# Kernel optimization log

Hardware: AMD Instinct MI355X
Metric: run time of the kernel (lower is better)

The kernel has to match this reference:

```python
import jax, jax.numpy as jnp
import numpy as np

L, B, S, D = 8, 1, 4096, 2048
H, KVH, HD = 16, 2, 128
Q = 32
THETA = 1e6
MROPE = (16, 24, 24)  # mrope_section, sums to HD//2
EPS = 1e-6


def setup_inputs() -> dict:
    key = jax.random.key(0)
    ks = jax.random.split(key, 8)
    hidden_states = jax.random.normal(ks[0], (L, B, S, D), dtype=jnp.float32)
    ln_w = jax.random.uniform(ks[1], (L, D), dtype=jnp.float32, minval=0.5, maxval=1.5)
    q_w = jax.random.normal(ks[2], (L, D, H * HD), dtype=jnp.float32) * 0.02
    q_b = jax.random.normal(ks[3], (L, H * HD), dtype=jnp.float32) * 0.02
    k_w = jax.random.normal(ks[4], (L, D, KVH * HD), dtype=jnp.float32) * 0.02
    k_b = jax.random.normal(ks[5], (L, KVH * HD), dtype=jnp.float32) * 0.02
    position_ids = jax.random.randint(ks[6], (3, B, S), 0, S, dtype=jnp.int32)
    q_idx = jnp.sort(jax.random.randint(ks[7], (Q,), 0, S, dtype=jnp.int32))
    return {"hidden_states": hidden_states, "ln_w": ln_w, "q_w": q_w, "q_b": q_b,
            "k_w": k_w, "k_b": k_b, "position_ids": position_ids, "q_idx": q_idx}


def _rot_half(x):
    h = x.shape[-1] // 2
    return jnp.concatenate([-x[..., h:], x[..., :h]], axis=-1)


def _mrope_combine(t):
    # t: (3, B, S, HD). Split last dim per 2*mrope_section, chunk i taken from axis i%3.
    parts, off = [], 0
    for i, sec in enumerate(MROPE):
        w = 2 * sec
        parts.append(t[i % 3, :, :, off:off + w])
        off += w
    return jnp.concatenate(parts, axis=-1)[:, None, :, :]  # (B, 1, S, HD)


def reference(hidden_states, ln_w, q_w, q_b, k_w, k_b, position_ids, q_idx):
    # Rotary embeddings from 3D mRoPE position ids
    inv_freq = 1.0 / (THETA ** (jnp.arange(0, HD, 2, dtype=jnp.float32) / HD))  # (HD/2,)
    freqs = position_ids.astype(jnp.float32)[..., None] * inv_freq  # (3, B, S, HD/2)
    emb = jnp.concatenate([freqs, freqs], axis=-1)  # (3, B, S, HD)
    cos = _mrope_combine(jnp.cos(emb))  # (B, 1, S, HD)
    sin = _mrope_combine(jnp.sin(emb))
    cos_q = cos[:, :, q_idx, :]  # (B, 1, Q, HD)
    sin_q = sin[:, :, q_idx, :]
    # Eager causal mask sliced at query rows: (Q, S)
    mask_add = jnp.where(jnp.arange(S)[None, :] > q_idx[:, None], -1e9, 0.0).astype(jnp.float32)

    scale = 1.0 / np.sqrt(HD).astype(np.float32)

    def per_layer(hs, lw, qw, qb, kw, kb):
        # RMSNorm (input_layernorm)
        var = jnp.mean(jnp.square(hs), axis=-1, keepdims=True)
        x = hs * jax.lax.rsqrt(var + EPS) * lw  # (B, S, D)
        xq = x[:, q_idx, :]  # (B, Q, D)
        k = (jnp.einsum('bsd,de->bse', x, kw) + kb).reshape(B, S, KVH, HD).transpose(0, 2, 1, 3)
        q = (jnp.einsum('bqd,de->bqe', xq, qw) + qb).reshape(B, Q, H, HD).transpose(0, 2, 1, 3)
        k = jnp.repeat(k, H // KVH, axis=1)  # repeat_kv -> (B, H, S, HD)
        k = k * cos + _rot_half(k) * sin
        q = q * cos_q + _rot_half(q) * sin_q
        scores = jnp.einsum('bhqd,bhkd->bhqk', q, k) * scale  # (B, H, Q, S)
        scores = scores + mask_add[None, None]
        return jax.nn.softmax(scores.astype(jnp.float32), axis=-1)

    return jax.vmap(per_layer)(hidden_states, ln_w, q_w, q_b, k_w, k_b)  # (L, B, H, Q, S)
```

## Files before the change

kernel.cpp:

```cpp
#include <hip/hip_runtime.h>
#include <hip/hip_bf16.h>
#include <math.h>

#define LYR 8
#define SEQ 4096
#define DIM 2048
#define NH 16
#define HD 128
#define NQ 32
#define NKV 256
#define NQE 2048

typedef __attribute__((ext_vector_type(8))) short short8;
typedef __attribute__((ext_vector_type(4))) float f32x4;

#define WS_IRQ   0
#define WS_ABLOB 256
#define WS_COS   524544
#define WS_SIN   1048832
#define WS_QBUF  1573120
#define WS_PART  2097408
#define WS_W2    4194560
#define WS_KBLOB 8388864
#define WS_QBLOB 16777472

__device__ __forceinline__ short f2bf(float x) {
  __hip_bfloat16 h = __float2bfloat16(x);
  return *(short*)&h;
}
__device__ __forceinline__ float bf2f(short s) {
  unsigned u = ((unsigned)(unsigned short)s) << 16;
  return __uint_as_float(u);
}

__device__ __forceinline__ void split1(float x, short& h, short& l) {
  unsigned b = __float_as_uint(x);
  h = (short)(b >> 16);
  float lo = x - __uint_as_float(b & 0xffff0000u);
  l = (short)((__float_as_uint(lo) + 0x8000u) >> 16);
}

#define GLOAD16(srcp, dstp) \
  __builtin_amdgcn_global_load_lds( \
      (const __attribute__((address_space(1))) unsigned int*)(srcp), \
      (__attribute__((address_space(3))) unsigned int*)(dstp), 16, 0, 0)

#define RBAR() asm volatile("s_waitcnt lgkmcnt(0)\n\ts_barrier" ::: "memory")

__global__ __launch_bounds__(256) void prep_kernel(
    const float* __restrict__ ln_w, const float* __restrict__ k_w,
    short* __restrict__ W2) {
  int kb = blockIdx.x, l = blockIdx.y, t = threadIdx.x;
  const float* kwl = k_w + (size_t)l * DIM * NKV;
  const float* lnl = ln_w + l * DIM;
  short* blob = W2 + (size_t)(l * 64 + kb) * 16384;
  #pragma unroll
  for (int i = 0; i < 4; ++i) {
    int p = t + i * 256;
    int fi = p >> 6, lane = p & 63;
    int n = fi * 16 + (lane & 15);
    int k0 = kb * 32 + (lane >> 4) * 8;
    short hi8[8], lo8[8];
    #pragma unroll
    for (int e = 0; e < 8; ++e) {
      float v = lnl[k0 + e] * kwl[(size_t)(k0 + e) * NKV + n];
      short h = f2bf(v);
      hi8[e] = h;
      lo8[e] = f2bf(v - bf2f(h));
    }
    *(short8*)(blob + p * 8) = *(short8*)hi8;
    *(short8*)(blob + 8192 + p * 8) = *(short8*)lo8;
  }
}

__global__ __launch_bounds__(256) void rmsq_kernel(const float* __restrict__ hs,
                                                   const int* __restrict__ q_idx,
                                                   float* __restrict__ irq) {
  int qi = blockIdx.x, l = blockIdx.y, t = threadIdx.x;
  int s = q_idx[qi];
  const float* row = hs + ((size_t)l * SEQ + s) * DIM;
  float4 v0 = *(const float4*)(row + t * 4);
  float4 v1 = *(const float4*)(row + t * 4 + 1024);
  float acc = v0.x*v0.x + v0.y*v0.y + v0.z*v0.z + v0.w*v0.w
            + v1.x*v1.x + v1.y*v1.y + v1.z*v1.z + v1.w*v1.w;
  #pragma unroll
  for (int off = 32; off >= 1; off >>= 1) acc += __shfl_down(acc, off);
  __shared__ float red[4];
  if ((t & 63) == 0) red[t >> 6] = acc;
  __syncthreads();
  if (t == 0) {
    float tot = red[0] + red[1] + red[2] + red[3];
    irq[l * NQ + qi] = rsqrtf(tot / (float)DIM + 1e-6f);
  }
}

__global__ void cossin_kernel(const int* __restrict__ pos_ids,
                              float* __restrict__ cost, float* __restrict__ sint) {
  int idx = blockIdx.x * 256 + threadIdx.x;
  int s = idx >> 7, d = idx & 127;
  int t = (d < 32) ? 0 : (d < 80 ? 1 : 2);
  int j = d & 63;
  double invf = pow(1000000.0, -(double)j / 64.0);
  double ph = (double)pos_ids[t * SEQ + s] * invf;
  cost[idx] = (float)cos(ph);
  sint[idx] = (float)sin(ph);
}

__global__ __launch_bounds__(256) void xqt_kernel(
    const float* __restrict__ hs, const float* __restrict__ ln_w,
    const int* __restrict__ q_idx, const float* __restrict__ irq,
    short* __restrict__ Ablob) {
  __shared__ int qix[32];
  __shared__ float qir[32];
  int l = blockIdx.x, t = threadIdx.x;
  if (t < 32) { qix[t] = q_idx[t]; qir[t] = irq[l * NQ + t]; }
  __syncthreads();
  int lane = t & 63, g4 = t >> 6;
  short* base = Ablob + (size_t)l * 131072;
  int row = lane & 15, kgl = lane >> 4;
  for (int i = 0; i < 64; ++i) {
    int group = g4 * 64 + i;
    int kb = group >> 2, half = (group >> 1) & 1, mf = group & 1;
    int r = row + mf * 16;
    int k0 = kb * 32 + kgl * 8;
    const float* src = hs + ((size_t)l * SEQ + qix[r]) * DIM + k0;
    const float* lnp = ln_w + l * DIM + k0;
    float ir = qir[r];
    float4 v0 = *(const float4*)src;
    float4 v1 = *(const float4*)(src + 4);
    float4 w0 = *(const float4*)lnp;
    float4 w1 = *(const float4*)(lnp + 4);
    float av[8] = {v0.x*w0.x, v0.y*w0.y, v0.z*w0.z, v0.w*w0.w,
                   v1.x*w1.x, v1.y*w1.y, v1.z*w1.z, v1.w*w1.w};
    short o8[8];
    #pragma unroll
    for (int e = 0; e < 8; ++e) {
      float v = av[e] * ir;
      short hh, ll;
      split1(v, hh, ll);
      o8[e] = half ? ll : hh;
    }
    *(short8*)(base + group * 512 + lane * 8) = *(short8*)o8;
  }
}

__global__ __launch_bounds__(256) void kgemm_kernel(
    const float* __restrict__ hs, const short* __restrict__ W2,
    const float* __restrict__ k_b, const float* __restrict__ cost,
    const float* __restrict__ sint, short* __restrict__ Kblob) {
  __shared__ __align__(1024) char SM[65536];

  int t = threadIdx.x;
  int fid = blockIdx.x;
  int l = fid & 7, sb = fid >> 3;
  int s0 = sb * 64;
  int lane = t & 63, w = t >> 6;
  int fr = lane & 15, kg = lane >> 4;
  int arow = t >> 2, akg = t & 3;

  const float* hrow = hs + ((size_t)l * SEQ + s0 + arow) * DIM + akg * 8;
  const char* wbase = (const char*)(W2 + (size_t)l * 64 * 16384);
  const char* wfrag = wbase + w * 1024 + lane * 16;

  int awoff = (arow >> 4) * 1024 + (((akg * 16 + (arow & 15)) * 16) ^ (akg << 5));
  int aroff = (lane * 16) ^ ((lane >> 4) << 5);

  f32x4 acc[4][4];
  #pragma unroll
  for (int mf = 0; mf < 4; ++mf)
    #pragma unroll
    for (int nf = 0; nf < 4; ++nf) acc[mf][nf] = (f32x4){0.f, 0.f, 0.f, 0.f};
  float sq = 0.f;
  float4 rA0, rA1, rB0, rB1;
  short8 B0h[4], B0l[4], B1h[4], B1l[4];

  {
    #pragma unroll
    for (int nf = 0; nf < 4; ++nf) {
      B0h[nf] = *(const short8*)(wfrag + nf * 4096);
      B0l[nf] = *(const short8*)(wfrag + nf * 4096 + 16384);
    }
    float4 a0 = *(const float4*)(hrow);
    float4 a1 = *(const float4*)(hrow + 4);
    float av[8] = {a0.x, a0.y, a0.z, a0.w, a1.x, a1.y, a1.z, a1.w};
    short hi8[8], lo8[8];
    #pragma unroll
    for (int e = 0; e < 8; ++e) {
      sq = fmaf(av[e], av[e], sq);
      split1(av[e], hi8[e], lo8[e]);
    }
    *(short8*)(SM + awoff) = *(short8*)hi8;
    *(short8*)(SM + 4096 + awoff) = *(short8*)lo8;
    rA0 = *(const float4*)(hrow + 32);
    rA1 = *(const float4*)(hrow + 36);
  }
  RBAR();

#define KSTEP8(KB, CA0, CA1, NA0, NA1, UBH, UBL, PBH, PBL) do { \
    int buf_ = (KB) & 1; \
    const char* asb_ = SM + buf_ * 8192; \
     \
    if ((KB) < 63) { \
      const char* bsrc_ = wfrag + (size_t)((KB) + 1) * 32768; \
      _Pragma("unroll") \
      for (int nf = 0; nf < 4; ++nf) { \
        PBH[nf] = *(const short8*)(bsrc_ + nf * 4096); \
        PBL[nf] = *(const short8*)(bsrc_ + nf * 4096 + 16384); \
      } \
    } \
    if ((KB) < 62) { \
      NA0 = *(const float4*)(hrow + ((KB) + 2) * 32); \
      NA1 = *(const float4*)(hrow + ((KB) + 2) * 32 + 4); \
    } \
    short8 ah_[4], al_[4]; \
    _Pragma("unroll") \
    for (int mf = 0; mf < 4; ++mf) { \
      ah_[mf] = *(const short8*)(asb_ + mf * 1024 + aroff); \
      al_[mf] = *(const short8*)(asb_ + 4096 + mf * 1024 + aroff); \
    } \
    __builtin_amdgcn_s_barrier(); \
    asm volatile("s_waitcnt lgkmcnt(0)" ::: "memory"); \
    __builtin_amdgcn_s_setprio(1); \
    _Pragma("unroll") \
    for (int nf = 0; nf < 2; ++nf) \
      _Pragma("unroll") \
      for (int mf = 0; mf < 4; ++mf) \
        acc[mf][nf] = __builtin_amdgcn_mfma_f32_16x16x32_bf16(ah_[mf], UBH[nf], acc[mf][nf], 0, 0, 0); \
    _Pragma("unroll") \
    for (int nf = 0; nf < 2; ++nf) \
      _Pragma("unroll") \
      for (int mf = 0; mf < 4; ++mf) \
        acc[mf][nf] = __builtin_amdgcn_mfma_f32_16x16x32_bf16(ah_[mf], UBL[nf], acc[mf][nf], 0, 0, 0); \
    _Pragma("unroll") \
    for (int nf = 0; nf < 2; ++nf) \
      _Pragma("unroll") \
      for (int mf = 0; mf < 4; ++mf) \
        acc[mf][nf] = __builtin_amdgcn_mfma_f32_16x16x32_bf16(al_[mf], UBH[nf], acc[mf][nf], 0, 0, 0); \
    __builtin_amdgcn_s_setprio(0); \
    __builtin_amdgcn_s_barrier(); \
     \
    if ((KB) < 63) { \
      char* asn_ = SM + (buf_ ^ 1) * 8192; \
      float av_[8] = {CA0.x, CA0.y, CA0.z, CA0.w, CA1.x, CA1.y, CA1.z, CA1.w}; \
      short hi8_[8], lo8_[8]; \
      _Pragma("unroll") \
      for (int e = 0; e < 8; ++e) { \
        sq = fmaf(av_[e], av_[e], sq); \
        split1(av_[e], hi8_[e], lo8_[e]); \
      } \
      *(short8*)(asn_ + awoff) = *(short8*)hi8_; \
      *(short8*)(asn_ + 4096 + awoff) = *(short8*)lo8_; \
    } \
    __builtin_amdgcn_s_setprio(1); \
    _Pragma("unroll") \
    for (int nf = 2; nf < 4; ++nf) \
      _Pragma("unroll") \
      for (int mf = 0; mf < 4; ++mf) \
        acc[mf][nf] = __builtin_amdgcn_mfma_f32_16x16x32_bf16(ah_[mf], UBH[nf], acc[mf][nf], 0, 0, 0); \
    _Pragma("unroll") \
    for (int nf = 2; nf < 4; ++nf) \
      _Pragma("unroll") \
      for (int mf = 0; mf < 4; ++mf) \
        acc[mf][nf] = __builtin_amdgcn_mfma_f32_16x16x32_bf16(ah_[mf], UBL[nf], acc[mf][nf], 0, 0, 0); \
    _Pragma("unroll") \
    for (int nf = 2; nf < 4; ++nf) \
      _Pragma("unroll") \
      for (int mf = 0; mf < 4; ++mf) \
        acc[mf][nf] = __builtin_amdgcn_mfma_f32_16x16x32_bf16(al_[mf], UBH[nf], acc[mf][nf], 0, 0, 0); \
    __builtin_amdgcn_s_setprio(0); \
    asm volatile("s_waitcnt lgkmcnt(0)" ::: "memory"); \
    __builtin_amdgcn_s_barrier(); \
  } while (0)

  for (int kb2 = 0; kb2 < 32; ++kb2) {
    KSTEP8(2 * kb2,     rA0, rA1, rB0, rB1, B0h, B0l, B1h, B1l);
    KSTEP8(2 * kb2 + 1, rB0, rB1, rA0, rA1, B1h, B1l, B0h, B0l);
  }
#undef KSTEP8

  sq += __shfl_xor(sq, 1);
  sq += __shfl_xor(sq, 2);
  float* smf = (float*)SM;
  __syncthreads();
  if ((t & 3) == 0) smf[arow] = sq;
  __syncthreads();
  float irv[16];
  #pragma unroll
  for (int mf = 0; mf < 4; ++mf)
    #pragma unroll
    for (int r = 0; r < 4; ++r)
      irv[mf * 4 + r] = rsqrtf(smf[mf * 16 + kg * 4 + r] / (float)DIM + 1e-6f);
  __syncthreads();

  float* Kraw = smf;
  int j = w * 16 + fr;
  float bias0 = k_b[l * NKV + j];
  float bias1 = k_b[l * NKV + j + 64];
  float bias2 = k_b[l * NKV + j + 128];
  float bias3 = k_b[l * NKV + j + 192];
  #pragma unroll
  for (int mf = 0; mf < 4; ++mf) {
    #pragma unroll
    for (int r = 0; r < 4; ++r) {
      int row = mf * 16 + kg * 4 + r;
      int s = s0 + row;
      float ir = irv[mf * 4 + r];
      float v0 = acc[mf][0][r] * ir + bias0;
      float v1 = acc[mf][1][r] * ir + bias1;
      float v2 = acc[mf][2][r] * ir + bias2;
      float v3 = acc[mf][3][r] * ir + bias3;
      float cj = cost[s * HD + j], sj = sint[s * HD + j];
      float cj2 = cost[s * HD + j + 64], sj2 = sint[s * HD + j + 64];
      int sw = (row & 7) << 2;
      float* kr = Kraw + row * 256;
      kr[j ^ sw]           = v0 * cj - v1 * sj;
      kr[(j + 64) ^ sw]    = v1 * cj2 + v0 * sj2;
      kr[(j + 128) ^ sw]   = v2 * cj - v3 * sj;
      kr[(j + 192) ^ sw]   = v3 * cj2 + v2 * sj2;
    }
  }
  __syncthreads();

  int kc = sb >> 1, fb = (sb & 1) * 4;
  #pragma unroll
  for (int i = 0; i < 8; ++i) {
    int c = t + i * 256;
    int lc = c & 63, fl = (c >> 6) & 3, ts2 = (c >> 8) & 3, kv = c >> 10;
    int key = fl * 16 + (lc & 15);
    int d0 = kv * 128 + ts2 * 32 + (lc >> 4) * 8;
    int sw = (key & 7) << 2;
    float4 x0 = *(const float4*)(Kraw + key * 256 + (d0 ^ sw));
    float4 x1 = *(const float4*)(Kraw + key * 256 + ((d0 + 4) ^ sw));
    float av[8] = {x0.x, x0.y, x0.z, x0.w, x1.x, x1.y, x1.z, x1.w};
    short hi8[8], lo8[8];
    #pragma unroll
    for (int e = 0; e < 8; ++e) split1(av[e], hi8[e], lo8[e]);
    short* bb = Kblob + (size_t)((l * 2 + kv) * 32 + kc) * 32768
              + (size_t)((ts2 * 2 + 0) * 8 + fb + fl) * 512 + lc * 8;
    *(short8*)bb = *(short8*)hi8;
    *(short8*)(bb + 4096) = *(short8*)lo8;
  }
}

__global__ __launch_bounds__(512) void qgemm_kernel(
    const float* __restrict__ q_w, const short* __restrict__ Ablob,
    float* __restrict__ part) {
  __shared__ __align__(1024) char SM[131072];
  int t = threadIdx.x;
  int nc = blockIdx.x, ks = blockIdx.y, l = blockIdx.z;
  int lane = t & 63, w = t >> 6;
  int fr = lane & 15, kg = lane >> 4;
  const char* abase = (const char*)(Ablob + (size_t)l * 131072 + (size_t)ks * 32768);
  const float* qwl = q_w + (size_t)l * DIM * NQE;

  #pragma unroll
  for (int c = 0; c < 8; ++c) {
    int chunk = w * 8 + c;
    GLOAD16(abase + chunk * 1024 + lane * 16, SM + chunk * 1024);
  }
  #pragma unroll
  for (int c = 0; c < 4; ++c) {
    int r = w * 4 + c;
    GLOAD16((const char*)(qwl + (size_t)(ks * 512 + r) * NQE + nc * 256) + lane * 16,
            SM + 65536 + r * 1024 + lane * 16);
  }
  f32x4 acc[2][2];
  #pragma unroll
  for (int mf = 0; mf < 2; ++mf)
    #pragma unroll
    for (int nf = 0; nf < 2; ++nf) acc[mf][nf] = (f32x4){0.f, 0.f, 0.f, 0.f};
  __syncthreads();

  for (int ts = 0; ts < 16; ++ts) {
    int buf = ts & 1;
    if (ts < 15) {
      #pragma unroll
      for (int c = 0; c < 4; ++c) {
        int r = w * 4 + c;
        GLOAD16((const char*)(qwl + (size_t)(ks * 512 + (ts + 1) * 32 + r) * NQE + nc * 256) + lane * 16,
                SM + 65536 + (buf ^ 1) * 32768 + r * 1024 + lane * 16);
      }
    }
    short8 ah[2], al[2];
    #pragma unroll
    for (int mf = 0; mf < 2; ++mf) {
      ah[mf] = *(const short8*)(SM + ts * 4096 + mf * 1024 + lane * 16);
      al[mf] = *(const short8*)(SM + ts * 4096 + 2048 + mf * 1024 + lane * 16);
    }
    const float* bt = (const float*)(SM + 65536 + buf * 32768);
    short8 bh[2], bl[2];
    #pragma unroll
    for (int nf = 0; nf < 2; ++nf) {
      int c = w * 32 + nf * 16 + fr;
      short bh8[8], bl8[8];
      #pragma unroll
      for (int e = 0; e < 8; ++e) {
        float v = bt[(kg * 8 + e) * 256 + c];
        split1(v, bh8[e], bl8[e]);
      }
      bh[nf] = *(short8*)bh8;
      bl[nf] = *(short8*)bl8;
    }
    #pragma unroll
    for (int nf = 0; nf < 2; ++nf)
      #pragma unroll
      for (int mf = 0; mf < 2; ++mf)
        acc[mf][nf] = __builtin_amdgcn_mfma_f32_16x16x32_bf16(ah[mf], bh[nf], acc[mf][nf], 0, 0, 0);
    #pragma unroll
    for (int nf = 0; nf < 2; ++nf)
      #pragma unroll
      for (int mf = 0; mf < 2; ++mf)
        acc[mf][nf] = __builtin_amdgcn_mfma_f32_16x16x32_bf16(ah[mf], bl[nf], acc[mf][nf], 0, 0, 0);
    #pragma unroll
    for (int nf = 0; nf < 2; ++nf)
      #pragma unroll
      for (int mf = 0; mf < 2; ++mf)
        acc[mf][nf] = __builtin_amdgcn_mfma_f32_16x16x32_bf16(al[mf], bh[nf], acc[mf][nf], 0, 0, 0);
    __syncthreads();
  }

  #pragma unroll
  for (int mf = 0; mf < 2; ++mf) {
    #pragma unroll
    for (int r = 0; r < 4; ++r) {
      int row = mf * 16 + kg * 4 + r;
      float* prow = part + ((size_t)((ks * LYR + l) * NQ + row)) * NQE + nc * 256;
      #pragma unroll
      for (int nf = 0; nf < 2; ++nf) {
        int col = w * 32 + nf * 16 + fr;
        prow[col] = acc[mf][nf][r];
      }
    }
  }
}

__global__ __launch_bounds__(256) void qred_kernel(
    const float* __restrict__ part, const float* __restrict__ q_b,
    float* __restrict__ Qbuf) {
  int idx = blockIdx.x * 256 + threadIdx.x;
  int n = idx & 2047, q = (idx >> 11) & 31, l = idx >> 16;
  float v = q_b[l * NQE + n];
  #pragma unroll
  for (int ks = 0; ks < 4; ++ks)
    v += part[((size_t)((ks * LYR + l) * NQ + q)) * NQE + n];
  Qbuf[((size_t)l * NQ + q) * NQE + n] = v;
}

__global__ __launch_bounds__(256) void qpack_kernel(
    const float* __restrict__ Qbuf, const float* __restrict__ cost,
    const float* __restrict__ sint, const int* __restrict__ q_idx,
    short* __restrict__ Qblob) {
  int kv = blockIdx.x, l = blockIdx.y, t = threadIdx.x;
  short* blob = Qblob + (size_t)(l * 2 + kv) * 65536;
  #pragma unroll
  for (int i = 0; i < 16; ++i) {
    int p = t + i * 256;
    int ts = p >> 10, f = (p >> 6) & 15, lane = p & 63;
    int row = f * 16 + (lane & 15);
    int hh = row >> 5, q = row & 31;
    int h = kv * 8 + hh;
    int d0 = ts * 32 + (lane >> 4) * 8;
    int s = q_idx[q];
    const float* qrow = Qbuf + ((size_t)l * NQ + q) * NQE + h * HD;
    const float* ct = cost + s * HD;
    const float* st = sint + s * HD;
    short hi8[8], lo8[8];
    #pragma unroll
    for (int e = 0; e < 8; ++e) {
      int d = d0 + e;
      float x = qrow[d];
      float xp = qrow[d ^ 64];
      float v = (d < 64) ? (x * ct[d] - xp * st[d]) : (x * ct[d] + xp * st[d]);
      split1(v, hi8[e], lo8[e]);
    }
    *(short8*)(blob + ((ts * 2 + 0) * 16 + f) * 512 + lane * 8) = *(short8*)hi8;
    *(short8*)(blob + ((ts * 2 + 1) * 16 + f) * 512 + lane * 8) = *(short8*)lo8;
  }
}

__global__ __launch_bounds__(512) void scores_kernel(
    const short* __restrict__ Qblob, const short* __restrict__ Kblob,
    const int* __restrict__ q_idx, float* __restrict__ out) {
  __shared__ short Qs[2][16384];
  __shared__ short Ks[2][8192];
  __shared__ int qiv[32];
  int t = threadIdx.x;
  int kc = blockIdx.x, kv = blockIdx.y, l = blockIdx.z;
  int lane = t & 63, w = t >> 6;
  int wm = w >> 1, wn = w & 1;
  if (t < 32) qiv[t] = q_idx[t];
  const char* qsrc = (const char*)(Qblob + (size_t)(l * 2 + kv) * 65536);
  const char* ksrc = (const char*)(Kblob + (size_t)((l * 2 + kv) * 32 + kc) * 32768);
  #pragma unroll
  for (int c = 0; c < 4; ++c) {
    int off = (w * 4 + c) * 1024;
    GLOAD16(qsrc + off + lane * 16, (char*)Qs[0] + off);
  }
  #pragma unroll
  for (int c = 0; c < 2; ++c) {
    int off = (w * 2 + c) * 1024;
    GLOAD16(ksrc + off + lane * 16, (char*)Ks[0] + off);
  }
  f32x4 acc[4][4];
  #pragma unroll
  for (int mf = 0; mf < 4; ++mf)
    #pragma unroll
    for (int nf = 0; nf < 4; ++nf) acc[mf][nf] = (f32x4){0.f, 0.f, 0.f, 0.f};
  __syncthreads();
  for (int ts = 0; ts < 4; ++ts) {
    int buf = ts & 1;
    if (ts < 3) {
      const char* qs = qsrc + (ts + 1) * 32768;
      const char* ks = ksrc + (ts + 1) * 16384;
      #pragma unroll
      for (int c = 0; c < 4; ++c) {
        int off = (w * 4 + c) * 1024;
        GLOAD16(qs + off + lane * 16, (char*)Qs[(ts + 1) & 1] + off);
      }
      #pragma unroll
      for (int c = 0; c < 2; ++c) {
        int off = (w * 2 + c) * 1024;
        GLOAD16(ks + off + lane * 16, (char*)Ks[(ts + 1) & 1] + off);
      }
    }
    short8 ah[4], al[4];
    #pragma unroll
    for (int mf = 0; mf < 4; ++mf) {
      int f = wm * 4 + mf;
      ah[mf] = *(const short8*)(Qs[buf] + f * 512 + lane * 8);
      al[mf] = *(const short8*)(Qs[buf] + 8192 + f * 512 + lane * 8);
    }
    short8 bh[4], bl[4];
    #pragma unroll
    for (int nf = 0; nf < 4; ++nf) {
      int f = wn * 4 + nf;
      bh[nf] = *(const short8*)(Ks[buf] + f * 512 + lane * 8);
      bl[nf] = *(const short8*)(Ks[buf] + 4096 + f * 512 + lane * 8);
    }
    #pragma unroll
    for (int nf = 0; nf < 4; ++nf)
      #pragma unroll
      for (int mf = 0; mf < 4; ++mf)
        acc[mf][nf] = __builtin_amdgcn_mfma_f32_16x16x32_bf16(ah[mf], bh[nf], acc[mf][nf], 0, 0, 0);
    #pragma unroll
    for (int nf = 0; nf < 4; ++nf)
      #pragma unroll
      for (int mf = 0; mf < 4; ++mf)
        acc[mf][nf] = __builtin_amdgcn_mfma_f32_16x16x32_bf16(ah[mf], bl[nf], acc[mf][nf], 0, 0, 0);
    #pragma unroll
    for (int nf = 0; nf < 4; ++nf)
      #pragma unroll
      for (int mf = 0; mf < 4; ++mf)
        acc[mf][nf] = __builtin_amdgcn_mfma_f32_16x16x32_bf16(al[mf], bh[nf], acc[mf][nf], 0, 0, 0);
    __syncthreads();
  }
  const float scale = 0.088388347648318447f;
  #pragma unroll
  for (int mf = 0; mf < 4; ++mf) {
    #pragma unroll
    for (int r = 0; r < 4; ++r) {
      int rr = wm * 64 + mf * 16 + (lane >> 4) * 4 + r;
      int hh = rr >> 5, q = rr & 31;
      int qv = qiv[q];
      float* orow = out + (((size_t)(l * NH + kv * 8 + hh)) * NQ + q) * SEQ;
      #pragma unroll
      for (int nf = 0; nf < 4; ++nf) {
        int key = kc * 128 + (wn * 4 + nf) * 16 + (lane & 15);
        orow[key] = (key > qv) ? -1e9f : acc[mf][nf][r] * scale;
      }
    }
  }
}

__global__ __launch_bounds__(256) void softmax_kernel(float* __restrict__ out) {
  size_t row = blockIdx.x;
  float* p = out + row * SEQ;
  int t = threadIdx.x;
  float4 v[4];
  float mx = -1e30f;
  #pragma unroll
  for (int i = 0; i < 4; ++i) {
    v[i] = *(const float4*)(p + t * 4 + i * 1024);
    mx = fmaxf(mx, fmaxf(fmaxf(v[i].x, v[i].y), fmaxf(v[i].z, v[i].w)));
  }
  #pragma unroll
  for (int off = 32; off >= 1; off >>= 1) mx = fmaxf(mx, __shfl_xor(mx, off));
  __shared__ float red[4];
  if ((t & 63) == 0) red[t >> 6] = mx;
  __syncthreads();
  mx = fmaxf(fmaxf(red[0], red[1]), fmaxf(red[2], red[3]));
  __syncthreads();
  float sum = 0.f;
  #pragma unroll
  for (int i = 0; i < 4; ++i) {
    v[i].x = __expf(v[i].x - mx); v[i].y = __expf(v[i].y - mx);
    v[i].z = __expf(v[i].z - mx); v[i].w = __expf(v[i].w - mx);
    sum += v[i].x + v[i].y + v[i].z + v[i].w;
  }
  #pragma unroll
  for (int off = 32; off >= 1; off >>= 1) sum += __shfl_xor(sum, off);
  if ((t & 63) == 0) red[t >> 6] = sum;
  __syncthreads();
  sum = red[0] + red[1] + red[2] + red[3];
  float inv = 1.f / sum;
  #pragma unroll
  for (int i = 0; i < 4; ++i) {
    v[i].x *= inv; v[i].y *= inv; v[i].z *= inv; v[i].w *= inv;
    *(float4*)(p + t * 4 + i * 1024) = v[i];
  }
}

extern "C" void kernel_launch(void* const* d_in, const int* in_sizes, int n_in,
                              void* d_out, int out_size, void* d_ws, size_t ws_size,
                              hipStream_t stream) {
  const float* hs   = (const float*)d_in[0];
  const float* ln_w = (const float*)d_in[1];
  const float* q_w  = (const float*)d_in[2];
  const float* q_b  = (const float*)d_in[3];
  const float* k_w  = (const float*)d_in[4];
  const float* k_b  = (const float*)d_in[5];
  const int* pos    = (const int*)d_in[6];
  const int* qidx   = (const int*)d_in[7];
  float* out = (float*)d_out;
  float* ws = (float*)d_ws;
  float* irq   = ws + WS_IRQ;
  short* Ablob = (short*)(ws + WS_ABLOB);
  float* cost  = ws + WS_COS;
  float* sint  = ws + WS_SIN;
  float* Qbuf  = ws + WS_QBUF;
  float* part  = ws + WS_PART;
  short* W2    = (short*)(ws + WS_W2);
  short* Kblob = (short*)(ws + WS_KBLOB);
  short* Qblob = (short*)(ws + WS_QBLOB);

  prep_kernel<<<dim3(64, LYR), 256, 0, stream>>>(ln_w, k_w, W2);
  rmsq_kernel<<<dim3(NQ, LYR), 256, 0, stream>>>(hs, qidx, irq);
  cossin_kernel<<<(SEQ * HD) / 256, 256, 0, stream>>>(pos, cost, sint);
  xqt_kernel<<<LYR, 256, 0, stream>>>(hs, ln_w, qidx, irq, Ablob);
  kgemm_kernel<<<512, 256, 0, stream>>>(hs, W2, k_b, cost, sint, Kblob);
  qgemm_kernel<<<dim3(8, 4, LYR), 512, 0, stream>>>(q_w, Ablob, part);
  qred_kernel<<<2048, 256, 0, stream>>>(part, q_b, Qbuf);
  qpack_kernel<<<dim3(2, LYR), 256, 0, stream>>>(Qbuf, cost, sint, qidx, Qblob);
  scores_kernel<<<dim3(32, 2, LYR), 512, 0, stream>>>(Qblob, Kblob, qidx, out);
  softmax_kernel<<<LYR * NH * NQ, 256, 0, stream>>>(out);
}
```

Measured before the change: 267.0 us.

## Fuse scores and softmax into one attention kernel, retile Q GEMM

Replaces the separate scores kernel (which wrote pre-softmax scores to global memory) and the softmax kernel (which read them back) with a single attention kernel. Each block computes the masked scores for 8 query rows of one head into LDS, then applies the softmax and writes the output once. This removes a full round trip of the large output tensor through HBM. The Q projection GEMM is also retiled into smaller blocks (256 threads, half the N and K per block, more blocks and more split-K partials), and Q RoPE plus scaling is done in fp32 instead of being packed into bf16 blobs. In exchange, the attention kernel wastes half of each MFMA on zero-padded rows, uses a large LDS buffer that limits occupancy, and reads K through a per-block XCD-aware mapping.

New measurement: 264.8 us. About the same (-0.8%).

```diff
diff --git a/kernel.cpp b/kernel.cpp
--- a/kernel.cpp
+++ b/kernel.cpp
@@ -20,9 +20,9 @@
 #define WS_SIN   1048832
 #define WS_QBUF  1573120
 #define WS_PART  2097408
-#define WS_W2    4194560
-#define WS_KBLOB 8388864
-#define WS_QBLOB 16777472
+#define WS_W2    6291712
+#define WS_KBLOB 10486016
+#define WS_QROPE 18874624
 
 __device__ __forceinline__ short f2bf(float x) {
   __hip_bfloat16 h = __float2bfloat16(x);
@@ -199,7 +199,6 @@
 #define KSTEP8(KB, CA0, CA1, NA0, NA1, UBH, UBL, PBH, PBL) do { \
     int buf_ = (KB) & 1; \
     const char* asb_ = SM + buf_ * 8192; \
-     \
     if ((KB) < 63) { \
       const char* bsrc_ = wfrag + (size_t)((KB) + 1) * 32768; \
       _Pragma("unroll") \
@@ -238,7 +237,6 @@
         acc[mf][nf] = __builtin_amdgcn_mfma_f32_16x16x32_bf16(al_[mf], UBH[nf], acc[mf][nf], 0, 0, 0); \
     __builtin_amdgcn_s_setprio(0); \
     __builtin_amdgcn_s_barrier(); \
-     \
     if ((KB) < 63) { \
       char* asn_ = SM + (buf_ ^ 1) * 8192; \
       float av_[8] = {CA0.x, CA0.y, CA0.z, CA0.w, CA1.x, CA1.y, CA1.z, CA1.w}; \
@@ -342,15 +340,15 @@
   }
 }
 
-__global__ __launch_bounds__(512) void qgemm_kernel(
+__global__ __launch_bounds__(256) void qgemm_kernel(
     const float* __restrict__ q_w, const short* __restrict__ Ablob,
     float* __restrict__ part) {
-  __shared__ __align__(1024) char SM[131072];
+  __shared__ __align__(1024) char SM[65536];
   int t = threadIdx.x;
   int nc = blockIdx.x, ks = blockIdx.y, l = blockIdx.z;
   int lane = t & 63, w = t >> 6;
   int fr = lane & 15, kg = lane >> 4;
-  const char* abase = (const char*)(Ablob + (size_t)l * 131072 + (size_t)ks * 32768);
+  const char* abase = (const char*)(Ablob + (size_t)l * 131072 + (size_t)ks * 16384);
   const float* qwl = q_w + (size_t)l * DIM * NQE;
 
   #pragma unroll
@@ -360,9 +358,9 @@
   }
   #pragma unroll
   for (int c = 0; c < 4; ++c) {
-    int r = w * 4 + c;
-    GLOAD16((const char*)(qwl + (size_t)(ks * 512 + r) * NQE + nc * 256) + lane * 16,
-            SM + 65536 + r * 1024 + lane * 16);
+    int r2 = (w * 4 + c) * 2;
+    const char* src = (const char*)(qwl + (size_t)(ks * 256 + r2 + (lane >> 5)) * NQE + nc * 128) + (lane & 31) * 16;
+    GLOAD16(src, SM + 32768 + (w * 4 + c) * 1024);
   }
   f32x4 acc[2][2];
   #pragma unroll
@@ -371,14 +369,14 @@
     for (int nf = 0; nf < 2; ++nf) acc[mf][nf] = (f32x4){0.f, 0.f, 0.f, 0.f};
   __syncthreads();
 
-  for (int ts = 0; ts < 16; ++ts) {
+  for (int ts = 0; ts < 8; ++ts) {
     int buf = ts & 1;
-    if (ts < 15) {
+    if (ts < 7) {
       #pragma unroll
       for (int c = 0; c < 4; ++c) {
-        int r = w * 4 + c;
-        GLOAD16((const char*)(qwl + (size_t)(ks * 512 + (ts + 1) * 32 + r) * NQE + nc * 256) + lane * 16,
-                SM + 65536 + (buf ^ 1) * 32768 + r * 1024 + lane * 16);
+        int r2 = (w * 4 + c) * 2;
+        const char* src = (const char*)(qwl + (size_t)(ks * 256 + (ts + 1) * 32 + r2 + (lane >> 5)) * NQE + nc * 128) + (lane & 31) * 16;
+        GLOAD16(src, SM + 32768 + (buf ^ 1) * 16384 + (w * 4 + c) * 1024);
       }
     }
     short8 ah[2], al[2];
@@ -387,7 +385,7 @@
       ah[mf] = *(const short8*)(SM + ts * 4096 + mf * 1024 + lane * 16);
       al[mf] = *(const short8*)(SM + ts * 4096 + 2048 + mf * 1024 + lane * 16);
     }
-    const float* bt = (const float*)(SM + 65536 + buf * 32768);
+    const float* bt = (const float*)(SM + 32768 + buf * 16384);
     short8 bh[2], bl[2];
     #pragma unroll
     for (int nf = 0; nf < 2; ++nf) {
@@ -395,7 +393,7 @@
       short bh8[8], bl8[8];
       #pragma unroll
       for (int e = 0; e < 8; ++e) {
-        float v = bt[(kg * 8 + e) * 256 + c];
+        float v = bt[(kg * 8 + e) * 128 + c];
         split1(v, bh8[e], bl8[e]);
       }
       bh[nf] = *(short8*)bh8;
@@ -424,7 +422,7 @@
     #pragma unroll
     for (int r = 0; r < 4; ++r) {
       int row = mf * 16 + kg * 4 + r;
-      float* prow = part + ((size_t)((ks * LYR + l) * NQ + row)) * NQE + nc * 256;
+      float* prow = part + ((size_t)((ks * LYR + l) * NQ + row)) * NQE + nc * 128;
       #pragma unroll
       for (int nf = 0; nf < 2; ++nf) {
         int col = w * 32 + nf * 16 + fr;
@@ -441,172 +439,142 @@
   int n = idx & 2047, q = (idx >> 11) & 31, l = idx >> 16;
   float v = q_b[l * NQE + n];
   #pragma unroll
-  for (int ks = 0; ks < 4; ++ks)
+  for (int ks = 0; ks < 8; ++ks)
     v += part[((size_t)((ks * LYR + l) * NQ + q)) * NQE + n];
   Qbuf[((size_t)l * NQ + q) * NQE + n] = v;
 }
 
-__global__ __launch_bounds__(256) void qpack_kernel(
+__global__ __launch_bounds__(256) void qrope_kernel(
     const float* __restrict__ Qbuf, const float* __restrict__ cost,
     const float* __restrict__ sint, const int* __restrict__ q_idx,
-    short* __restrict__ Qblob) {
-  int kv = blockIdx.x, l = blockIdx.y, t = threadIdx.x;
-  short* blob = Qblob + (size_t)(l * 2 + kv) * 65536;
-  #pragma unroll
-  for (int i = 0; i < 16; ++i) {
-    int p = t + i * 256;
-    int ts = p >> 10, f = (p >> 6) & 15, lane = p & 63;
-    int row = f * 16 + (lane & 15);
-    int hh = row >> 5, q = row & 31;
-    int h = kv * 8 + hh;
-    int d0 = ts * 32 + (lane >> 4) * 8;
-    int s = q_idx[q];
-    const float* qrow = Qbuf + ((size_t)l * NQ + q) * NQE + h * HD;
-    const float* ct = cost + s * HD;
-    const float* st = sint + s * HD;
-    short hi8[8], lo8[8];
-    #pragma unroll
-    for (int e = 0; e < 8; ++e) {
-      int d = d0 + e;
-      float x = qrow[d];
-      float xp = qrow[d ^ 64];
-      float v = (d < 64) ? (x * ct[d] - xp * st[d]) : (x * ct[d] + xp * st[d]);
-      split1(v, hi8[e], lo8[e]);
-    }
-    *(short8*)(blob + ((ts * 2 + 0) * 16 + f) * 512 + lane * 8) = *(short8*)hi8;
-    *(short8*)(blob + ((ts * 2 + 1) * 16 + f) * 512 + lane * 8) = *(short8*)lo8;
-  }
-}
-
-__global__ __launch_bounds__(512) void scores_kernel(
-    const short* __restrict__ Qblob, const short* __restrict__ Kblob,
+    float* __restrict__ Qrope) {
+  int p = blockIdx.x * 256 + threadIdx.x;
+  int j = p & 63, q = (p >> 6) & 31, h = (p >> 11) & 15, l = p >> 15;
+  int s = q_idx[q];
+  const float* qrow = Qbuf + ((size_t)l * NQ + q) * NQE + h * HD;
+  float x1 = qrow[j], x2 = qrow[j + 64];
+  float c1 = cost[s * HD + j],      s1 = sint[s * HD + j];
+  float c2 = cost[s * HD + j + 64], s2 = sint[s * HD + j + 64];
+  const float SC = 0.088388347648318447f;
+  float* orow = Qrope + ((size_t)(l * NH + h) * NQ + q) * HD;
+  orow[j]      = (x1 * c1 - x2 * s1) * SC;
+  orow[j + 64] = (x2 * c2 + x1 * s2) * SC;
+}
+
+__global__ __launch_bounds__(512) void attn_kernel(
+    const float* __restrict__ Qrope, const short* __restrict__ Kblob,
     const int* __restrict__ q_idx, float* __restrict__ out) {
-  __shared__ short Qs[2][16384];
-  __shared__ short Ks[2][8192];
-  __shared__ int qiv[32];
+  __shared__ float smS[8 * 4104];
+  __shared__ int qiv8[8];
   int t = threadIdx.x;
-  int kc = blockIdx.x, kv = blockIdx.y, l = blockIdx.z;
+  int bid = blockIdx.x;
+  int xcd = bid & 7, idx = bid >> 3;
+  int pp = 2 * xcd + (idx >> 5);
+  int l = pp >> 1, kv = pp & 1;
+  int hh = (idx >> 2) & 7, qg = idx & 3;
+  int h = kv * 8 + hh;
+  int q0 = qg * 8;
   int lane = t & 63, w = t >> 6;
-  int wm = w >> 1, wn = w & 1;
-  if (t < 32) qiv[t] = q_idx[t];
-  const char* qsrc = (const char*)(Qblob + (size_t)(l * 2 + kv) * 65536);
-  const char* ksrc = (const char*)(Kblob + (size_t)((l * 2 + kv) * 32 + kc) * 32768);
-  #pragma unroll
-  for (int c = 0; c < 4; ++c) {
-    int off = (w * 4 + c) * 1024;
-    GLOAD16(qsrc + off + lane * 16, (char*)Qs[0] + off);
-  }
-  #pragma unroll
-  for (int c = 0; c < 2; ++c) {
-    int off = (w * 2 + c) * 1024;
-    GLOAD16(ksrc + off + lane * 16, (char*)Ks[0] + off);
-  }
-  f32x4 acc[4][4];
-  #pragma unroll
-  for (int mf = 0; mf < 4; ++mf)
-    #pragma unroll
-    for (int nf = 0; nf < 4; ++nf) acc[mf][nf] = (f32x4){0.f, 0.f, 0.f, 0.f};
-  __syncthreads();
+  int g = lane >> 4;
+
+  if (t < 8) qiv8[t] = q_idx[q0 + t];
+
+  short8 Ah[4], Al[4];
+  {
+    int arow = lane & 15, akg = lane >> 4;
+    if (arow < 8) {
+      const float* qr = Qrope + ((size_t)(l * NH + h) * NQ + q0 + arow) * HD + akg * 8;
+      #pragma unroll
+      for (int ts = 0; ts < 4; ++ts) {
+        float4 a0 = *(const float4*)(qr + ts * 32);
+        float4 a1 = *(const float4*)(qr + ts * 32 + 4);
+        float av[8] = {a0.x, a0.y, a0.z, a0.w, a1.x, a1.y, a1.z, a1.w};
+        short hi8[8], lo8[8];
+        #pragma unroll
+        for (int e = 0; e < 8; ++e) split1(av[e], hi8[e], lo8[e]);
+        Ah[ts] = *(short8*)hi8;
+        Al[ts] = *(short8*)lo8;
+      }
+    } else {
+      short z8[8] = {0, 0, 0, 0, 0, 0, 0, 0};
+      #pragma unroll
+      for (int ts = 0; ts < 4; ++ts) { Ah[ts] = *(short8*)z8; Al[ts] = *(short8*)z8; }
+    }
+  }
+  const short* kbase = Kblob + (size_t)((l * 2 + kv) * 32) * 32768 + w * 512 + lane * 8;
+  short8 K0h[4], K0l[4], K1h[4], K1l[4];
+  #pragma unroll
   for (int ts = 0; ts < 4; ++ts) {
-    int buf = ts & 1;
-    if (ts < 3) {
-      const char* qs = qsrc + (ts + 1) * 32768;
-      const char* ks = ksrc + (ts + 1) * 16384;
-      #pragma unroll
-      for (int c = 0; c < 4; ++c) {
-        int off = (w * 4 + c) * 1024;
-        GLOAD16(qs + off + lane * 16, (char*)Qs[(ts + 1) & 1] + off);
-      }
-      #pragma unroll
-      for (int c = 0; c < 2; ++c) {
-        int off = (w * 2 + c) * 1024;
-        GLOAD16(ks + off + lane * 16, (char*)Ks[(ts + 1) & 1] + off);
-      }
-    }
-    short8 ah[4], al[4];
-    #pragma unroll
-    for (int mf = 0; mf < 4; ++mf) {
-      int f = wm * 4 + mf;
-      ah[mf] = *(const short8*)(Qs[buf] + f * 512 + lane * 8);
-      al[mf] = *(const short8*)(Qs[buf] + 8192 + f * 512 + lane * 8);
-    }
-    short8 bh[4], bl[4];
-    #pragma unroll
-    for (int nf = 0; nf < 4; ++nf) {
-      int f = wn * 4 + nf;
-      bh[nf] = *(const short8*)(Ks[buf] + f * 512 + lane * 8);
-      bl[nf] = *(const short8*)(Ks[buf] + 4096 + f * 512 + lane * 8);
-    }
-    #pragma unroll
-    for (int nf = 0; nf < 4; ++nf)
-      #pragma unroll
-      for (int mf = 0; mf < 4; ++mf)
-        acc[mf][nf] = __builtin_amdgcn_mfma_f32_16x16x32_bf16(ah[mf], bh[nf], acc[mf][nf], 0, 0, 0);
-    #pragma unroll
-    for (int nf = 0; nf < 4; ++nf)
-      #pragma unroll
-      for (int mf = 0; mf < 4; ++mf)
-        acc[mf][nf] = __builtin_amdgcn_mfma_f32_16x16x32_bf16(ah[mf], bl[nf], acc[mf][nf], 0, 0, 0);
-    #pragma unroll
-    for (int nf = 0; nf < 4; ++nf)
-      #pragma unroll
-      for (int mf = 0; mf < 4; ++mf)
-        acc[mf][nf] = __builtin_amdgcn_mfma_f32_16x16x32_bf16(al[mf], bh[nf], acc[mf][nf], 0, 0, 0);
-    __syncthreads();
-  }
-  const float scale = 0.088388347648318447f;
-  #pragma unroll
-  for (int mf = 0; mf < 4; ++mf) {
-    #pragma unroll
-    for (int r = 0; r < 4; ++r) {
-      int rr = wm * 64 + mf * 16 + (lane >> 4) * 4 + r;
-      int hh = rr >> 5, q = rr & 31;
-      int qv = qiv[q];
-      float* orow = out + (((size_t)(l * NH + kv * 8 + hh)) * NQ + q) * SEQ;
-      #pragma unroll
-      for (int nf = 0; nf < 4; ++nf) {
-        int key = kc * 128 + (wn * 4 + nf) * 16 + (lane & 15);
-        orow[key] = (key > qv) ? -1e9f : acc[mf][nf][r] * scale;
-      }
-    }
-  }
-}
-
-__global__ __launch_bounds__(256) void softmax_kernel(float* __restrict__ out) {
-  size_t row = blockIdx.x;
-  float* p = out + row * SEQ;
-  int t = threadIdx.x;
-  float4 v[4];
+    K0h[ts] = *(const short8*)(kbase + ts * 8192);
+    K0l[ts] = *(const short8*)(kbase + ts * 8192 + 4096);
+  }
+  __syncthreads();
+
+#define ACHUNK(KC, CH, CL, NH_, NL_) do { \
+    if ((KC) < 31) { \
+      const short* nb = kbase + (size_t)((KC) + 1) * 32768; \
+      _Pragma("unroll") \
+      for (int ts = 0; ts < 4; ++ts) { \
+        NH_[ts] = *(const short8*)(nb + ts * 8192); \
+        NL_[ts] = *(const short8*)(nb + ts * 8192 + 4096); \
+      } \
+    } \
+    f32x4 acc = (f32x4){0.f, 0.f, 0.f, 0.f}; \
+    _Pragma("unroll") \
+    for (int ts = 0; ts < 4; ++ts) \
+      acc = __builtin_amdgcn_mfma_f32_16x16x32_bf16(Ah[ts], CH[ts], acc, 0, 0, 0); \
+    _Pragma("unroll") \
+    for (int ts = 0; ts < 4; ++ts) \
+      acc = __builtin_amdgcn_mfma_f32_16x16x32_bf16(Ah[ts], CL[ts], acc, 0, 0, 0); \
+    _Pragma("unroll") \
+    for (int ts = 0; ts < 4; ++ts) \
+      acc = __builtin_amdgcn_mfma_f32_16x16x32_bf16(Al[ts], CH[ts], acc, 0, 0, 0); \
+    if (g < 2) { \
+      int key = (KC) * 128 + w * 16 + (lane & 15); \
+      _Pragma("unroll") \
+      for (int rr = 0; rr < 4; ++rr) { \
+        int r8 = g * 4 + rr; \
+        float v = (key > qiv8[r8]) ? -1e9f : acc[rr]; \
+        smS[r8 * 4104 + key] = v; \
+      } \
+    } \
+  } while (0)
+
+  for (int kc2 = 0; kc2 < 16; ++kc2) {
+    ACHUNK(2 * kc2,     K0h, K0l, K1h, K1l);
+    ACHUNK(2 * kc2 + 1, K1h, K1l, K0h, K0l);
+  }
+#undef ACHUNK
+
+  __syncthreads();
+  int srow = w;
+  float* S = smS + srow * 4104;
   float mx = -1e30f;
   #pragma unroll
-  for (int i = 0; i < 4; ++i) {
-    v[i] = *(const float4*)(p + t * 4 + i * 1024);
-    mx = fmaxf(mx, fmaxf(fmaxf(v[i].x, v[i].y), fmaxf(v[i].z, v[i].w)));
+  for (int c = 0; c < 16; ++c) {
+    float4 x = *(const float4*)(S + c * 256 + lane * 4);
+    mx = fmaxf(mx, fmaxf(fmaxf(x.x, x.y), fmaxf(x.z, x.w)));
   }
   #pragma unroll
   for (int off = 32; off >= 1; off >>= 1) mx = fmaxf(mx, __shfl_xor(mx, off));
-  __shared__ float red[4];
-  if ((t & 63) == 0) red[t >> 6] = mx;
-  __syncthreads();
-  mx = fmaxf(fmaxf(red[0], red[1]), fmaxf(red[2], red[3]));
-  __syncthreads();
   float sum = 0.f;
   #pragma unroll
-  for (int i = 0; i < 4; ++i) {
-    v[i].x = __expf(v[i].x - mx); v[i].y = __expf(v[i].y - mx);
-    v[i].z = __expf(v[i].z - mx); v[i].w = __expf(v[i].w - mx);
-    sum += v[i].x + v[i].y + v[i].z + v[i].w;
+  for (int c = 0; c < 16; ++c) {
+    float4 x = *(const float4*)(S + c * 256 + lane * 4);
+    x.x = __expf(x.x - mx); x.y = __expf(x.y - mx);
+    x.z = __expf(x.z - mx); x.w = __expf(x.w - mx);
+    sum += x.x + x.y + x.z + x.w;
+    *(float4*)(S + c * 256 + lane * 4) = x;
   }
   #pragma unroll
   for (int off = 32; off >= 1; off >>= 1) sum += __shfl_xor(sum, off);
-  if ((t & 63) == 0) red[t >> 6] = sum;
-  __syncthreads();
-  sum = red[0] + red[1] + red[2] + red[3];
   float inv = 1.f / sum;
-  #pragma unroll
-  for (int i = 0; i < 4; ++i) {
-    v[i].x *= inv; v[i].y *= inv; v[i].z *= inv; v[i].w *= inv;
-    *(float4*)(p + t * 4 + i * 1024) = v[i];
+  float* orow = out + ((size_t)(l * NH + h) * NQ + q0 + srow) * SEQ;
+  #pragma unroll
+  for (int c = 0; c < 16; ++c) {
+    float4 x = *(const float4*)(S + c * 256 + lane * 4);
+    x.x *= inv; x.y *= inv; x.z *= inv; x.w *= inv;
+    *(float4*)(orow + c * 256 + lane * 4) = x;
   }
 }
 
@@ -631,16 +599,15 @@
   float* part  = ws + WS_PART;
   short* W2    = (short*)(ws + WS_W2);
   short* Kblob = (short*)(ws + WS_KBLOB);
-  short* Qblob = (short*)(ws + WS_QBLOB);
+  float* Qrope = ws + WS_QROPE;
 
   prep_kernel<<<dim3(64, LYR), 256, 0, stream>>>(ln_w, k_w, W2);
   rmsq_kernel<<<dim3(NQ, LYR), 256, 0, stream>>>(hs, qidx, irq);
   cossin_kernel<<<(SEQ * HD) / 256, 256, 0, stream>>>(pos, cost, sint);
   xqt_kernel<<<LYR, 256, 0, stream>>>(hs, ln_w, qidx, irq, Ablob);
   kgemm_kernel<<<512, 256, 0, stream>>>(hs, W2, k_b, cost, sint, Kblob);
-  qgemm_kernel<<<dim3(8, 4, LYR), 512, 0, stream>>>(q_w, Ablob, part);
+  qgemm_kernel<<<dim3(16, 8, LYR), 256, 0, stream>>>(q_w, Ablob, part);
   qred_kernel<<<2048, 256, 0, stream>>>(part, q_b, Qbuf);
-  qpack_kernel<<<dim3(2, LYR), 256, 0, stream>>>(Qbuf, cost, sint, qidx, Qblob);
-  scores_kernel<<<dim3(32, 2, LYR), 512, 0, stream>>>(Qblob, Kblob, qidx, out);
-  softmax_kernel<<<LYR * NH * NQ, 256, 0, stream>>>(out);
-}
+  qrope_kernel<<<1024, 256, 0, stream>>>(Qbuf, cost, sint, qidx, Qrope);
+  attn_kernel<<<512, 512, 0, stream>>>(Qrope, Kblob, qidx, out);
+}
```
